# Optimization experiments

Measured on AMD Instinct MI355X. Metric: run time of the kernel, lower is better.

The kernel has to match this reference:

```python
import jax, jax.numpy as jnp
import numpy as np
from jax import lax

ROUTINGS = 3
SCALING = 2
NUM_CAPSULE = 8
NUM_ATOMS = 16
EPS = 1e-9


def squash(v):
    # SegCaps squash: v * |v|^2 / ((1+|v|^2) * |v|), norm over last axis
    sq = jnp.sum(v * v, axis=-1, keepdims=True)
    return v * sq / ((1.0 + sq) * jnp.sqrt(sq + EPS))


def setup_inputs() -> dict:
    key = jax.random.key(0)
    k1, k2 = jax.random.split(key)
    B, H, Wd, Cin, Ain = 4, 56, 56, 8, 32
    x = jax.random.normal(k1, (B, H, Wd, Cin, Ain), dtype=jnp.float32)
    # TF conv2d_transpose filter layout: [k, k, out_ch, in_ch]
    W = jax.random.normal(k2, (4, 4, NUM_CAPSULE * NUM_ATOMS, Ain), dtype=jnp.float32) * 0.05
    b = 0.1 * jnp.ones((1, 1, NUM_CAPSULE, NUM_ATOMS), dtype=jnp.float32)
    return {"x": x, "W": W, "b": b}


def reference(x, W, b):
    B, H, Wd, Cin, Ain = x.shape
    Cout, Aout = NUM_CAPSULE, NUM_ATOMS
    # [B,H,W,Cin,A] -> [Cin,B,H,W,A] -> [Cin*B,H,W,A]  (faithful to original ordering)
    xt = jnp.transpose(x, (3, 0, 1, 2, 4)).reshape(Cin * B, H, Wd, Ain)
    # TF conv2d_transpose, SAME padding, stride=scaling: out spatial = in * scaling
    out = lax.conv_transpose(
        xt, W, strides=(SCALING, SCALING), padding="SAME",
        dimension_numbers=("NHWC", "HWIO", "NHWC"), transpose_kernel=True)
    Hp, Wp = out.shape[1], out.shape[2]
    # votes: [B, Cin, Hp, Wp, Cout, Aout]  (faithful to original reshape)
    votes = out.reshape(B, Cin, Hp, Wp, Cout, Aout)
    biases = jnp.broadcast_to(b, (Hp, Wp, Cout, Aout))
    logits = jnp.zeros((B, Cin, Hp, Wp, Cout), dtype=x.dtype)
    act = None
    for i in range(ROUTINGS):
        route = jax.nn.softmax(logits, axis=-1)                      # [B,Cin,Hp,Wp,Cout]
        pre = jnp.einsum("bihwc,bihwca->bhwca", route, votes) + biases
        act = squash(pre)                                            # [B,Hp,Wp,Cout,Aout]
        if i < ROUTINGS - 1:
            logits = logits + jnp.einsum("bihwca,bhwca->bihwc", votes, act)
    return act
```

## Files before the change

### kernel.cpp

```cpp
#include <hip/hip_runtime.h>
#include <math.h>

#define CEPS 1e-9f

typedef _Float16 half8 __attribute__((ext_vector_type(8)));
typedef float floatx16 __attribute__((ext_vector_type(16)));


template<int CTRL>
__device__ __forceinline__ float dpp_add(float v) {
    return v + __int_as_float(__builtin_amdgcn_update_dpp(
        0, __float_as_int(v), CTRL, 0xF, 0xF, false));
}

__device__ __forceinline__ float sum_i8(float v) {
    v = dpp_add<0xB1>(v);
    v = dpp_add<0x4E>(v);
    v = dpp_add<0x141>(v);
    return v;
}

__device__ __forceinline__ float4 sel4(bool c, float4 a, float4 b) {
    return make_float4(c ? a.x : b.x, c ? a.y : b.y, c ? a.z : b.z, c ? a.w : b.w);
}

__global__ __launch_bounds__(256) void prep_w(const float* __restrict__ Wt,
                                              _Float16* __restrict__ wb) {
    int idx = blockIdx.x * 256 + threadIdx.x;
    int parity = idx >> 11;
    int s = (idx >> 8) & 7;
    int t = (idx >> 6) & 3;
    int l = idx & 63;
    int rh = parity >> 1, rw = parity & 1;
    int n = t * 32 + (l & 31);
    int h = l >> 5;
    int ci0 = ((s & 1) << 4) + (h << 3);
    int kh = ((s >> 2) << 1) + 1 - rh;
    int kw = (((s >> 1) & 1) << 1) + 1 - rw;
    const float* src = Wt + (((kh * 4 + kw) * 128 + n) << 5) + ci0;
    float4 w0 = *(const float4*)src;
    float4 w1 = *(const float4*)(src + 4);
    half8 hv;
    hv[0] = (_Float16)w0.x; hv[1] = (_Float16)w0.y;
    hv[2] = (_Float16)w0.z; hv[3] = (_Float16)w0.w;
    hv[4] = (_Float16)w1.x; hv[5] = (_Float16)w1.y;
    hv[6] = (_Float16)w1.z; hv[7] = (_Float16)w1.w;
    *(half8*)(wb + ((long)idx << 3)) = hv;
}

__global__ __launch_bounds__(256, 4) void caps_mfma(
    const float* __restrict__ x,
    const _Float16* __restrict__ wb,
    const float* __restrict__ bias,
    float* __restrict__ out)
{
    __shared__ _Float16 xt[25 * 8 * 40];
    __shared__ float scx[4][1152];
    __shared__ float bsh[136];

    const int tid = threadIdx.x;
    const int tile = blockIdx.x;
    const int tu = tile / 14, tv = tile - tu * 14;
    const int u0 = tu * 4, v0 = tv * 4;
    const int rh = blockIdx.y >> 1;
    const int rw = blockIdx.y & 1;
    const int bp = blockIdx.z;
    const _Float16* wsrc = wb + ((long)blockIdx.y << 14);

    if (tid < 128) bsh[(tid >> 4) * 17 + (tid & 15)] = bias[tid];

    #pragma unroll
    for (int it = 0; it < 4; ++it) {
        int idx = tid + (it << 8);
        if (idx < 800) {
            int cell = idx >> 5;
            int r = idx & 31;
            int i = r >> 2;
            int ci0 = (r & 3) << 3;
            int ri = cell / 5, rj = cell - ri * 5;
            int gi = u0 + rh - 1 + ri;
            int gj = v0 + rw - 1 + rj;
            float tmp[8] = {0.f, 0.f, 0.f, 0.f, 0.f, 0.f, 0.f, 0.f};
            if ((unsigned)gi < 56u && (unsigned)gj < 56u) {
                const float* src = x + (((i & 3) * 56 + gi) * 56 + gj) * 256
                                     + ((bp * 2 + (i >> 2)) << 5) + ci0;
                float4 a0 = *(const float4*)src;
                float4 a1 = *(const float4*)(src + 4);
                tmp[0] = a0.x; tmp[1] = a0.y; tmp[2] = a0.z; tmp[3] = a0.w;
                tmp[4] = a1.x; tmp[5] = a1.y; tmp[6] = a1.z; tmp[7] = a1.w;
            }
            half8 hv;
            #pragma unroll
            for (int j = 0; j < 8; ++j) hv[j] = (_Float16)tmp[j];
            *(half8*)(xt + (cell * 8 + i) * 40 + ci0) = hv;
        }
    }
    __syncthreads();

    const int l = tid & 63;
    const int w = tid >> 6;
    const int col = l & 31, h = l >> 5;
    const int invA = (l & 31) * 40 + (h << 3);

    floatx16 acc[4];
    #pragma unroll
    for (int t = 0; t < 4; ++t)
        #pragma unroll
        for (int j = 0; j < 16; ++j) acc[t][j] = 0.f;

    #pragma unroll
    for (int s = 0; s < 8; ++s) {
        const int tkh = s >> 2;
        const int tkw = (s >> 1) & 1;
        const int row = w + 1 - tkh;
        const int aoff = (row * 5 + 1 - tkw) * 320 + ((s & 1) << 4) + invA;
        half8 af = *(const half8*)(xt + aoff);
        #pragma unroll
        for (int t = 0; t < 4; ++t) {
            half8 bf = *(const half8*)(wsrc + (((s * 4 + t) * 64 + l) << 3));
            acc[t] = __builtin_amdgcn_mfma_f32_32x32x16_f16(af, bf, acc[t], 0, 0, 0);
        }
    }

    float* scb = &scx[w][0];
    const int cI = l >> 3;
    const int iI = l & 7;

    #pragma unroll
    for (int pixl = 0; pixl < 4; ++pixl) {
        #pragma unroll
        for (int t = 0; t < 4; ++t)
            #pragma unroll
            for (int il = 0; il < 4; ++il)
                scb[(t * 32 + col) * 9 + (h << 2) + il] = acc[t][pixl * 4 + il];
        float va[16];
        #pragma unroll
        for (int a = 0; a < 16; ++a) va[a] = scb[(cI * 16 + a) * 9 + iI];
        float4 bq[4];
        #pragma unroll
        for (int t = 0; t < 4; ++t) bq[t] = *(const float4*)(bsh + cI * 17 + t * 4);

        float pre[16], lg = 0.f;

        #pragma unroll
        for (int a = 0; a < 16; ++a) {
            float s = sum_i8(va[a]);
            pre[a] = fmaf(0.125f, s, (&bq[a >> 2].x)[a & 3]);
        }
        {
            float nq = pre[0] * pre[0];
            #pragma unroll
            for (int a = 1; a < 16; ++a) nq = fmaf(pre[a], pre[a], nq);
            float sc = nq * __builtin_amdgcn_rcpf(1.f + nq)
                          * __builtin_amdgcn_rsqf(nq + CEPS);
            #pragma unroll
            for (int a = 0; a < 16; ++a) pre[a] *= sc;
            float d = va[0] * pre[0];
            #pragma unroll
            for (int a = 1; a < 16; ++a) d = fmaf(va[a], pre[a], d);
            lg = d;
        }

        #pragma unroll
        for (int r = 1; r < 3; ++r) {
            float e = __expf(lg);
            float ss = dpp_add<0x128>(e);
            ss += __shfl_xor(ss, 16);
            ss += __shfl_xor(ss, 32);
            float route = e * __builtin_amdgcn_rcpf(ss);
            #pragma unroll
            for (int a = 0; a < 16; ++a) {
                float m = sum_i8(route * va[a]);
                pre[a] = m + (&bq[a >> 2].x)[a & 3];
            }
            float nq = pre[0] * pre[0];
            #pragma unroll
            for (int a = 1; a < 16; ++a) nq = fmaf(pre[a], pre[a], nq);
            float sc = nq * __builtin_amdgcn_rcpf(1.f + nq)
                          * __builtin_amdgcn_rsqf(nq + CEPS);
            #pragma unroll
            for (int a = 0; a < 16; ++a) pre[a] *= sc;
            if (r < 2) {
                float d = va[0] * pre[0];
                #pragma unroll
                for (int a = 1; a < 16; ++a) d = fmaf(va[a], pre[a], d);
                lg += d;
            }
        }

        float4 q0 = make_float4(pre[0],  pre[1],  pre[2],  pre[3]);
        float4 q1 = make_float4(pre[4],  pre[5],  pre[6],  pre[7]);
        float4 q2 = make_float4(pre[8],  pre[9],  pre[10], pre[11]);
        float4 q3 = make_float4(pre[12], pre[13], pre[14], pre[15]);
        float4 t0 = sel4((iI & 1) != 0, q1, q0);
        float4 t1 = sel4((iI & 1) != 0, q3, q2);
        float4 o4 = sel4((iI & 2) != 0, t1, t0);
        if (iI < 4) {
            const int p = ((u0 + w) << 1) + rh;
            const int q = ((v0 + pixl) << 1) + rw;
            *(float4*)(out + (((bp * 112 + p) * 112 + q) << 7) + cI * 16 + iI * 4) = o4;
        }
    }
}

extern "C" void kernel_launch(void* const* d_in, const int* in_sizes, int n_in,
                              void* d_out, int out_size, void* d_ws, size_t ws_size,
                              hipStream_t stream) {
    const float* x  = (const float*)d_in[0];
    const float* Wt = (const float*)d_in[1];
    const float* b  = (const float*)d_in[2];
    float* out = (float*)d_out;
    _Float16* wb = (_Float16*)d_ws;

    prep_w<<<32, 256, 0, stream>>>(Wt, wb);
    dim3 grid(196, 4, 4);
    caps_mfma<<<grid, 256, 0, stream>>>(x, wb, b, out);
}
```

Measured before the change: 128.1 us.

## Run capsule routing epilogue in packed fp16 with vectorized LDS reads

```diff
diff --git a/kernel.cpp b/kernel.cpp
--- a/kernel.cpp
+++ b/kernel.cpp
@@ -4,7 +4,10 @@
 #define CEPS 1e-9f
 
 typedef _Float16 half8 __attribute__((ext_vector_type(8)));
+typedef _Float16 h2 __attribute__((ext_vector_type(2)));
+typedef __fp16 fp16x2 __attribute__((ext_vector_type(2)));
 typedef float floatx16 __attribute__((ext_vector_type(16)));
+typedef float f32x4v __attribute__((ext_vector_type(4)));
 
 
 template<int CTRL>
@@ -12,16 +15,28 @@
     return v + __int_as_float(__builtin_amdgcn_update_dpp(
         0, __float_as_int(v), CTRL, 0xF, 0xF, false));
 }
-
-__device__ __forceinline__ float sum_i8(float v) {
-    v = dpp_add<0xB1>(v);
-    v = dpp_add<0x4E>(v);
-    v = dpp_add<0x141>(v);
+template<int CTRL>
+__device__ __forceinline__ h2 dpp_add_h2(h2 v) {
+    int t = __builtin_amdgcn_update_dpp(
+        0, __builtin_bit_cast(int, v), CTRL, 0xF, 0xF, false);
+    return v + __builtin_bit_cast(h2, t);
+}
+__device__ __forceinline__ h2 sum_i8_h2(h2 v) {
+    v = dpp_add_h2<0xB1>(v);
+    v = dpp_add_h2<0x4E>(v);
+    v = dpp_add_h2<0x141>(v);
     return v;
 }
-
-__device__ __forceinline__ float4 sel4(bool c, float4 a, float4 b) {
-    return make_float4(c ? a.x : b.x, c ? a.y : b.y, c ? a.z : b.z, c ? a.w : b.w);
+__device__ __forceinline__ h2 pkrtz(float a, float b) {
+    return __builtin_bit_cast(h2, __builtin_amdgcn_cvt_pkrtz(a, b));
+}
+__device__ __forceinline__ float fdot2(h2 a, h2 b, float c) {
+    return __builtin_amdgcn_fdot2(__builtin_bit_cast(fp16x2, a),
+                                  __builtin_bit_cast(fp16x2, b), c, false);
+}
+__device__ __forceinline__ h2 hsel(bool c, h2 a, h2 b) {
+    int r = c ? __builtin_bit_cast(int, a) : __builtin_bit_cast(int, b);
+    return __builtin_bit_cast(h2, r);
 }
 
 __global__ __launch_bounds__(256) void prep_w(const float* __restrict__ Wt,
@@ -55,8 +70,7 @@
     float* __restrict__ out)
 {
     __shared__ _Float16 xt[25 * 8 * 40];
-    __shared__ float scx[4][1152];
-    __shared__ float bsh[136];
+    __shared__ float scx[4][1056];
 
     const int tid = threadIdx.x;
     const int tile = blockIdx.x;
@@ -66,8 +80,6 @@
     const int rw = blockIdx.y & 1;
     const int bp = blockIdx.z;
     const _Float16* wsrc = wb + ((long)blockIdx.y << 14);
-
-    if (tid < 128) bsh[(tid >> 4) * 17 + (tid & 15)] = bias[tid];
 
     #pragma unroll
     for (int it = 0; it < 4; ++it) {
@@ -126,38 +138,59 @@
     const int cI = l >> 3;
     const int iI = l & 7;
 
+    h2 bq2[8];
+    {
+        const float* bpt = bias + (cI << 4);
+        float4 b0 = *(const float4*)bpt;
+        float4 b1 = *(const float4*)(bpt + 4);
+        float4 b2 = *(const float4*)(bpt + 8);
+        float4 b3 = *(const float4*)(bpt + 12);
+        bq2[0] = pkrtz(b0.x, b0.y); bq2[1] = pkrtz(b0.z, b0.w);
+        bq2[2] = pkrtz(b1.x, b1.y); bq2[3] = pkrtz(b1.z, b1.w);
+        bq2[4] = pkrtz(b2.x, b2.y); bq2[5] = pkrtz(b2.z, b2.w);
+        bq2[6] = pkrtz(b3.x, b3.y); bq2[7] = pkrtz(b3.z, b3.w);
+    }
+    const h2 c0125 = pkrtz(0.125f, 0.125f);
+
     #pragma unroll
     for (int pixl = 0; pixl < 4; ++pixl) {
         #pragma unroll
         for (int t = 0; t < 4; ++t)
             #pragma unroll
             for (int il = 0; il < 4; ++il)
-                scb[(t * 32 + col) * 9 + (h << 2) + il] = acc[t][pixl * 4 + il];
-        float va[16];
-        #pragma unroll
-        for (int a = 0; a < 16; ++a) va[a] = scb[(cI * 16 + a) * 9 + iI];
-        float4 bq[4];
-        #pragma unroll
-        for (int t = 0; t < 4; ++t) bq[t] = *(const float4*)(bsh + cI * 17 + t * 4);
-
-        float pre[16], lg = 0.f;
-
-        #pragma unroll
-        for (int a = 0; a < 16; ++a) {
-            float s = sum_i8(va[a]);
-            pre[a] = fmaf(0.125f, s, (&bq[a >> 2].x)[a & 3]);
+                scb[((h << 2) + il) * 132 + t * 32 + col] = acc[t][pixl * 4 + il];
+
+        const float* rb = scb + iI * 132 + (cI << 4);
+        f32x4v vq0 = *(const f32x4v*)(rb);
+        f32x4v vq1 = *(const f32x4v*)(rb + 4);
+        f32x4v vq2 = *(const f32x4v*)(rb + 8);
+        f32x4v vq3 = *(const f32x4v*)(rb + 12);
+        h2 va2[8];
+        va2[0] = pkrtz(vq0.x, vq0.y); va2[1] = pkrtz(vq0.z, vq0.w);
+        va2[2] = pkrtz(vq1.x, vq1.y); va2[3] = pkrtz(vq1.z, vq1.w);
+        va2[4] = pkrtz(vq2.x, vq2.y); va2[5] = pkrtz(vq2.z, vq2.w);
+        va2[6] = pkrtz(vq3.x, vq3.y); va2[7] = pkrtz(vq3.z, vq3.w);
+
+        h2 pre2[8];
+        float lg;
+
+        #pragma unroll
+        for (int j = 0; j < 8; ++j) {
+            h2 s2 = sum_i8_h2(va2[j]);
+            pre2[j] = s2 * c0125 + bq2[j];
         }
         {
-            float nq = pre[0] * pre[0];
-            #pragma unroll
-            for (int a = 1; a < 16; ++a) nq = fmaf(pre[a], pre[a], nq);
+            float nq = fdot2(pre2[0], pre2[0], 0.f);
+            #pragma unroll
+            for (int j = 1; j < 8; ++j) nq = fdot2(pre2[j], pre2[j], nq);
             float sc = nq * __builtin_amdgcn_rcpf(1.f + nq)
                           * __builtin_amdgcn_rsqf(nq + CEPS);
-            #pragma unroll
-            for (int a = 0; a < 16; ++a) pre[a] *= sc;
-            float d = va[0] * pre[0];
-            #pragma unroll
-            for (int a = 1; a < 16; ++a) d = fmaf(va[a], pre[a], d);
+            h2 sc2 = pkrtz(sc, sc);
+            #pragma unroll
+            for (int j = 0; j < 8; ++j) pre2[j] *= sc2;
+            float d = fdot2(va2[0], pre2[0], 0.f);
+            #pragma unroll
+            for (int j = 1; j < 8; ++j) d = fdot2(va2[j], pre2[j], d);
             lg = d;
         }
 
@@ -165,37 +198,41 @@
         for (int r = 1; r < 3; ++r) {
             float e = __expf(lg);
             float ss = dpp_add<0x128>(e);
-            ss += __shfl_xor(ss, 16);
+            ss += __int_as_float(__builtin_amdgcn_ds_swizzle(
+                      __float_as_int(ss), 0x401F));
             ss += __shfl_xor(ss, 32);
             float route = e * __builtin_amdgcn_rcpf(ss);
-            #pragma unroll
-            for (int a = 0; a < 16; ++a) {
-                float m = sum_i8(route * va[a]);
-                pre[a] = m + (&bq[a >> 2].x)[a & 3];
+            h2 rt2 = pkrtz(route, route);
+            #pragma unroll
+            for (int j = 0; j < 8; ++j) {
+                h2 p = sum_i8_h2(rt2 * va2[j]);
+                pre2[j] = p + bq2[j];
             }
-            float nq = pre[0] * pre[0];
-            #pragma unroll
-            for (int a = 1; a < 16; ++a) nq = fmaf(pre[a], pre[a], nq);
+            float nq = fdot2(pre2[0], pre2[0], 0.f);
+            #pragma unroll
+            for (int j = 1; j < 8; ++j) nq = fdot2(pre2[j], pre2[j], nq);
             float sc = nq * __builtin_amdgcn_rcpf(1.f + nq)
                           * __builtin_amdgcn_rsqf(nq + CEPS);
-            #pragma unroll
-            for (int a = 0; a < 16; ++a) pre[a] *= sc;
+            h2 sc2 = pkrtz(sc, sc);
+            #pragma unroll
+            for (int j = 0; j < 8; ++j) pre2[j] *= sc2;
             if (r < 2) {
-                float d = va[0] * pre[0];
+                float d = lg;
                 #pragma unroll
-                for (int a = 1; a < 16; ++a) d = fmaf(va[a], pre[a], d);
-                lg += d;
+                for (int j = 0; j < 8; ++j) d = fdot2(va2[j], pre2[j], d);
+                lg = d;
             }
         }
 
-        float4 q0 = make_float4(pre[0],  pre[1],  pre[2],  pre[3]);
-        float4 q1 = make_float4(pre[4],  pre[5],  pre[6],  pre[7]);
-        float4 q2 = make_float4(pre[8],  pre[9],  pre[10], pre[11]);
-        float4 q3 = make_float4(pre[12], pre[13], pre[14], pre[15]);
-        float4 t0 = sel4((iI & 1) != 0, q1, q0);
-        float4 t1 = sel4((iI & 1) != 0, q3, q2);
-        float4 o4 = sel4((iI & 2) != 0, t1, t0);
         if (iI < 4) {
+            h2 h0 = hsel((iI & 2) != 0, pre2[4], pre2[0]);
+            h2 h1 = hsel((iI & 2) != 0, pre2[5], pre2[1]);
+            h2 h2_ = hsel((iI & 2) != 0, pre2[6], pre2[2]);
+            h2 h3 = hsel((iI & 2) != 0, pre2[7], pre2[3]);
+            h2 p0 = hsel((iI & 1) != 0, h2_, h0);
+            h2 p1 = hsel((iI & 1) != 0, h3, h1);
+            float4 o4 = make_float4((float)p0.x, (float)p0.y,
+                                    (float)p1.x, (float)p1.y);
             const int p = ((u0 + w) << 1) + rh;
             const int q = ((v0 + pixl) << 1) + rw;
             *(float4*)(out + (((bp * 112 + p) * 112 + q) << 7) + cI * 16 + iI * 4) = o4;
```

Result: faster. 115.2 us (-10.1%).
